# Kernel optimization log

Measured on AMD Instinct MI355X. Metric: run time of the kernel, lower is better.

The kernel has to match this reference:

```python
import jax, jax.numpy as jnp
import numpy as np

N_USERS = 100_000
N_ITEMS = 50_000
N_EDGES = 2_000_000
D = 64
ALPHA = 0.5      # tanh-blend coefficient (alpha)
NORM_2 = -1.0    # exponent on back-aggregation degree norm (args.norm_2)


def setup_inputs() -> dict:
    key = jax.random.key(0)
    k1, k2, k3, k4, k5 = jax.random.split(key, 5)
    return {
        "h_user": jax.random.normal(k1, (N_USERS, D), jnp.float32) * 0.1,
        "pretrained_feature": jax.random.normal(k2, (N_ITEMS, D), jnp.float32),
        "edge_w": jax.random.normal(k3, (N_ITEMS, 1), jnp.float32),
        "src_idx": jax.random.randint(k4, (N_EDGES,), 0, N_USERS, dtype=jnp.int32),
        "dst_idx": jax.random.randint(k5, (N_EDGES,), 0, N_ITEMS, dtype=jnp.int32),
    }


def reference(h_user, pretrained_feature, edge_w, src_idx, dst_idx):
    # HGCNLayer.forward: bidirectional copy_src+sum aggregation with degree norm,
    # tanh prompt blend and node-softmax edge weighting.
    ones = jnp.ones((N_EDGES,), h_user.dtype)

    # forward pass user -> item: rst[d] = sum_{(s,d) in E} h_user[s]
    rst = jax.ops.segment_sum(h_user[src_idx], dst_idx, num_segments=N_ITEMS)  # [N_ITEMS, D]
    deg_dst = jnp.clip(jax.ops.segment_sum(ones, dst_idx, num_segments=N_ITEMS), 1.0)

    # alpha * tanh prompt blend
    rst = rst + ALPHA * jnp.tanh(pretrained_feature)
    # edge-prompt softmax scaling (softmax over nodes; see notes)
    rst = jax.nn.softmax(edge_w, axis=0) * rst
    # in-degree^-1 normalization
    rst = rst / deg_dst[:, None]

    # backward pass item -> user: bsrc[s] = sum_{(s,d) in E} rst[d]
    bsrc = jax.ops.segment_sum(rst[dst_idx], src_idx, num_segments=N_USERS)  # [N_USERS, D]
    deg_src = jnp.clip(jax.ops.segment_sum(ones, src_idx, num_segments=N_USERS), 1.0)
    bsrc = bsrc * jnp.power(deg_src, NORM_2)[:, None]
    return bsrc
```

## Files before the change

### kernel.cpp

```cpp
#include <hip/hip_runtime.h>
#include <hip/hip_bf16.h>
#include <math.h>

#define N_USERS 100000
#define N_ITEMS 50000
#define N_EDGES 2000000
#define D 64

#define FB_BINS 98
#define BB_BINS 196
#define NBINS   (FB_BINS + BB_BINS)
#define CHUNK   2048
#define NCHUNK  ((N_EDGES + CHUNK - 1) / CHUNK)
#define FWD_WGS 782
#define BWD_WGS 1563
#define CAP     4032

__device__ __forceinline__ float blo(unsigned u) {
    union { unsigned i; float f; } c; c.i = u << 16; return c.f;
}
__device__ __forceinline__ float bhi(unsigned u) {
    union { unsigned i; float f; } c; c.i = u & 0xFFFF0000u; return c.f;
}
__device__ __forceinline__ unsigned bpack(float x, float y) {
    __hip_bfloat16 a = __float2bfloat16(x), b = __float2bfloat16(y);
    unsigned short ua = *reinterpret_cast<unsigned short*>(&a);
    unsigned short ub = *reinterpret_cast<unsigned short*>(&b);
    return (unsigned)ua | ((unsigned)ub << 16);
}

__global__ __launch_bounds__(256) void h2b_kernel(
    const float2* __restrict__ in, unsigned* __restrict__ out, int n) {
    int stride = gridDim.x * blockDim.x;
    for (int i = blockIdx.x * blockDim.x + threadIdx.x; i < n; i += stride) {
        float2 v = in[i];
        out[i] = bpack(v.x, v.y);
    }
}

__global__ __launch_bounds__(256) void hist_kernel(
    const int* __restrict__ src, const int* __restrict__ dst, int* __restrict__ gh) {
    __shared__ int h[NBINS];
    for (int i = threadIdx.x; i < NBINS; i += 256) h[i] = 0;
    __syncthreads();
    int stride = gridDim.x * blockDim.x;
    for (int e = blockIdx.x * blockDim.x + threadIdx.x; e < N_EDGES; e += stride) {
        atomicAdd(&h[dst[e] >> 9], 1);
        atomicAdd(&h[FB_BINS + (src[e] >> 9)], 1);
    }
    __syncthreads();
    for (int i = threadIdx.x; i < NBINS; i += 256) {
        int v = h[i];
        if (v) atomicAdd(&gh[i], v);
    }
}

__global__ void scan_excl(const int* __restrict__ in, int* __restrict__ out,
                          int* __restrict__ cur, int n) {
    const int T = 1024, E = 4;
    __shared__ int wsum[16];
    __shared__ int s_carry;
    if (threadIdx.x == 0) s_carry = 0;
    __syncthreads();

    int lane = threadIdx.x & 63;
    int wid  = threadIdx.x >> 6;

    for (int base = 0; base < n; base += T * E) {
        int idx0 = base + threadIdx.x * E;
        int v[E];
        int tot = 0;
#pragma unroll
        for (int e = 0; e < E; e++) {
            int i = idx0 + e;
            v[e] = (i < n) ? in[i] : 0;
            tot += v[e];
        }
        int incl = tot;
#pragma unroll
        for (int off = 1; off < 64; off <<= 1) {
            int t = __shfl_up(incl, off);
            if (lane >= off) incl += t;
        }
        if (lane == 63) wsum[wid] = incl;
        __syncthreads();
        if (wid == 0 && lane < 16) {
            int t = wsum[lane];
            int sc = t;
#pragma unroll
            for (int off = 1; off < 16; off <<= 1) {
                int u = __shfl_up(sc, off);
                if (lane >= off) sc += u;
            }
            wsum[lane] = sc - t;
        }
        __syncthreads();
        int wave_off = wsum[wid];
        int excl = s_carry + wave_off + incl - tot;
#pragma unroll
        for (int e = 0; e < E; e++) {
            int i = idx0 + e;
            if (i < n) { out[i] = excl; cur[i] = excl; }
            excl += v[e];
        }
        __syncthreads();
        if (threadIdx.x == T - 1) s_carry += wave_off + incl;
        __syncthreads();
    }
    if (threadIdx.x == 0) out[n] = s_carry;
}

__global__ __launch_bounds__(256) void binfill_kernel(
    const int* __restrict__ src, const int* __restrict__ dst,
    int* __restrict__ gcur, unsigned* __restrict__ stage) {
    __shared__ int cnt[NBINS];
    __shared__ int gbase[NBINS];
    __shared__ int lcur[NBINS];
    int c = blockIdx.x;
    int base = c * CHUNK;
    int nEdge = N_EDGES - base; if (nEdge > CHUNK) nEdge = CHUNK;

    for (int t = threadIdx.x; t < NBINS; t += 256) { cnt[t] = 0; lcur[t] = 0; }
    __syncthreads();

    int es[8], ed[8];
#pragma unroll
    for (int j = 0; j < 8; j++) {
        int k = j * 256 + threadIdx.x;
        if (k < nEdge) {
            es[j] = src[base + k];
            ed[j] = dst[base + k];
            atomicAdd(&cnt[ed[j] >> 9], 1);
            atomicAdd(&cnt[FB_BINS + (es[j] >> 9)], 1);
        } else {
            es[j] = -1;
        }
    }
    __syncthreads();
    for (int t = threadIdx.x; t < NBINS; t += 256) {
        int cv = cnt[t];
        gbase[t] = cv ? atomicAdd(&gcur[t], cv) : 0;
    }
    __syncthreads();
#pragma unroll
    for (int j = 0; j < 8; j++) {
        if (es[j] >= 0) {
            int s = es[j], d = ed[j];
            int bf = d >> 9;
            int p = atomicAdd(&lcur[bf], 1);
            stage[gbase[bf] + p] = (unsigned)s | ((unsigned)(d & 511) << 17);
            int bb = FB_BINS + (s >> 9);
            int q = atomicAdd(&lcur[bb], 1);
            stage[gbase[bb] + q] = (unsigned)d | ((unsigned)(s & 511) << 16);
        }
    }
}

__global__ void softmax_stats_kernel(const float* __restrict__ w, float* __restrict__ stats) {
    __shared__ float red[16];
    int tid = threadIdx.x, lane = tid & 63, wid = tid >> 6;

    float m = -INFINITY;
    for (int i = tid; i < N_ITEMS; i += 1024) m = fmaxf(m, w[i]);
#pragma unroll
    for (int off = 32; off; off >>= 1) m = fmaxf(m, __shfl_xor(m, off));
    if (lane == 0) red[wid] = m;
    __syncthreads();
    if (tid == 0) {
        float t = red[0];
        for (int k = 1; k < 16; k++) t = fmaxf(t, red[k]);
        red[0] = t;
    }
    __syncthreads();
    m = red[0];
    __syncthreads();

    float s = 0.f;
    for (int i = tid; i < N_ITEMS; i += 1024) s += expf(w[i] - m);
#pragma unroll
    for (int off = 32; off; off >>= 1) s += __shfl_xor(s, off);
    if (lane == 0) red[wid] = s;
    __syncthreads();
    if (tid == 0) {
        float t = 0.f;
        for (int k = 0; k < 16; k++) t += red[k];
        stats[0] = m;
        stats[1] = t;
    }
}

__global__ __launch_bounds__(512) void pass2_fwd_kernel(
    const unsigned* __restrict__ hu16, const float* __restrict__ pf,
    const float* __restrict__ edge_w, const unsigned* __restrict__ stage,
    const int* __restrict__ binoff, const float* __restrict__ stats,
    unsigned* __restrict__ rst16) {
    __shared__ int cnt[64];
    __shared__ int loc[65];
    __shared__ int lcur[64];
    __shared__ int sorted[CAP];
    int r = blockIdx.x;
    int B = r >> 3, sub = r & 7;
    int beg = binoff[B], end = binoff[B + 1];
    int tid = threadIdx.x, lane = tid & 63, wv = tid >> 6;
    int q = lane & 31, half = lane >> 5;

    if (tid < 64) { cnt[tid] = 0; lcur[tid] = 0; }
    __syncthreads();

    for (int k = beg + tid; k < end; k += 512) {
        unsigned e = stage[k];
        if ((int)(e >> 23) == sub) atomicAdd(&cnt[(e >> 17) & 63], 1);
    }
    __syncthreads();
    if (tid < 64) {
        int v = cnt[tid];
        int incl = v;
#pragma unroll
        for (int off = 1; off < 64; off <<= 1) {
            int t = __shfl_up(incl, off);
            if (tid >= off) incl += t;
        }
        loc[tid] = incl - v;
        if (tid == 63) loc[64] = incl;
    }
    __syncthreads();
    int nf = loc[64];

    float m = stats[0], ssum = stats[1];
    const float2* PF2 = (const float2*)pf;

    if (nf <= CAP) {
        for (int k = beg + tid; k < end; k += 512) {
            unsigned e = stage[k];
            if ((int)(e >> 23) == sub) {
                int il = (e >> 17) & 63;
                int p = atomicAdd(&lcur[il], 1);
                sorted[loc[il] + p] = (int)(e & 0x1FFFFu);
            }
        }
        __syncthreads();
        for (int il = wv; il < 64; il += 8) {
            int i = r * 64 + il;
            if (i >= N_ITEMS) continue;
            int a = loc[il], b = loc[il + 1];
            float ax = 0.f, ay = 0.f;
            int k = a;
            for (; k + 8 <= b; k += 8) {
                int s0 = sorted[k + half],     s1 = sorted[k + 2 + half];
                int s2 = sorted[k + 4 + half], s3 = sorted[k + 6 + half];
                unsigned u0 = hu16[(s0 << 5) + q];
                unsigned u1 = hu16[(s1 << 5) + q];
                unsigned u2 = hu16[(s2 << 5) + q];
                unsigned u3 = hu16[(s3 << 5) + q];
                ax += (blo(u0) + blo(u1)) + (blo(u2) + blo(u3));
                ay += (bhi(u0) + bhi(u1)) + (bhi(u2) + bhi(u3));
            }
            for (; k + 2 <= b; k += 2) {
                unsigned u = hu16[(sorted[k + half] << 5) + q];
                ax += blo(u); ay += bhi(u);
            }
            if (k < b && half == 0) {
                unsigned u = hu16[(sorted[k] << 5) + q];
                ax += blo(u); ay += bhi(u);
            }
            ax += __shfl_xor(ax, 32);
            ay += __shfl_xor(ay, 32);
            if (half == 0) {
                float deg = (float)(b - a);
                if (deg < 1.f) deg = 1.f;
                float sc = expf(edge_w[i] - m) / (ssum * deg);
                float2 pv = PF2[(size_t)i * 32 + q];
                float vx = (ax + 0.5f * tanhf(pv.x)) * sc;
                float vy = (ay + 0.5f * tanhf(pv.y)) * sc;
                rst16[(size_t)i * 32 + q] = bpack(vx, vy);
            }
        }
    } else {
        const unsigned short* HU = (const unsigned short*)hu16;
        for (int il = wv; il < 64; il += 8) {
            int i = r * 64 + il;
            if (i >= N_ITEMS) continue;
            unsigned want = ((unsigned)sub << 6) | (unsigned)il;
            float acc = 0.f;
            int dcount = 0;
            for (int k = beg; k < end; k++) {
                unsigned e = stage[k];
                if ((e >> 17) == want) {
                    union { unsigned u; float f; } c;
                    c.u = (unsigned)HU[(size_t)(e & 0x1FFFFu) * 64 + lane] << 16;
                    acc += c.f; dcount++;
                }
            }
            float deg = (float)dcount;
            if (deg < 1.f) deg = 1.f;
            float sc = expf(edge_w[i] - m) / (ssum * deg);
            float val = (acc + 0.5f * tanhf(pf[(size_t)i * D + lane])) * sc;
            float va = __shfl(val, 2 * q);
            float vb = __shfl(val, 2 * q + 1);
            if (half == 0) rst16[(size_t)i * 32 + q] = bpack(va, vb);
        }
    }
}

__global__ __launch_bounds__(512) void pass2_bwd_kernel(
    const unsigned* __restrict__ rst16, const unsigned* __restrict__ stage,
    const int* __restrict__ binoff, float* __restrict__ out) {
    __shared__ int cnt[64];
    __shared__ int loc[65];
    __shared__ int lcur[64];
    __shared__ int sorted[CAP];
    int r = blockIdx.x;
    int B = FB_BINS + (r >> 3), sub = r & 7;
    int beg = binoff[B], end = binoff[B + 1];
    int tid = threadIdx.x, lane = tid & 63, wv = tid >> 6;
    int q = lane & 31, half = lane >> 5;

    if (tid < 64) { cnt[tid] = 0; lcur[tid] = 0; }
    __syncthreads();

    for (int k = beg + tid; k < end; k += 512) {
        unsigned e = stage[k];
        if ((int)(e >> 22) == sub) atomicAdd(&cnt[(e >> 16) & 63], 1);
    }
    __syncthreads();
    if (tid < 64) {
        int v = cnt[tid];
        int incl = v;
#pragma unroll
        for (int off = 1; off < 64; off <<= 1) {
            int t = __shfl_up(incl, off);
            if (tid >= off) incl += t;
        }
        loc[tid] = incl - v;
        if (tid == 63) loc[64] = incl;
    }
    __syncthreads();
    int nf = loc[64];

    float2* OUT2 = (float2*)out;

    if (nf <= CAP) {
        for (int k = beg + tid; k < end; k += 512) {
            unsigned e = stage[k];
            if ((int)(e >> 22) == sub) {
                int il = (e >> 16) & 63;
                int p = atomicAdd(&lcur[il], 1);
                sorted[loc[il] + p] = (int)(e & 0xFFFFu);
            }
        }
        __syncthreads();
        for (int il = wv; il < 64; il += 8) {
            int u = r * 64 + il;
            if (u >= N_USERS) continue;
            int a = loc[il], b = loc[il + 1];
            float ax = 0.f, ay = 0.f;
            int k = a;
            for (; k + 8 <= b; k += 8) {
                int d0 = sorted[k + half],     d1 = sorted[k + 2 + half];
                int d2 = sorted[k + 4 + half], d3 = sorted[k + 6 + half];
                unsigned u0 = rst16[(d0 << 5) + q];
                unsigned u1 = rst16[(d1 << 5) + q];
                unsigned u2 = rst16[(d2 << 5) + q];
                unsigned u3 = rst16[(d3 << 5) + q];
                ax += (blo(u0) + blo(u1)) + (blo(u2) + blo(u3));
                ay += (bhi(u0) + bhi(u1)) + (bhi(u2) + bhi(u3));
            }
            for (; k + 2 <= b; k += 2) {
                unsigned e = rst16[(sorted[k + half] << 5) + q];
                ax += blo(e); ay += bhi(e);
            }
            if (k < b && half == 0) {
                unsigned e = rst16[(sorted[k] << 5) + q];
                ax += blo(e); ay += bhi(e);
            }
            ax += __shfl_xor(ax, 32);
            ay += __shfl_xor(ay, 32);
            if (half == 0) {
                float deg = (float)(b - a);
                if (deg < 1.f) deg = 1.f;
                OUT2[(size_t)u * 32 + q] = make_float2(ax / deg, ay / deg);
            }
        }
    } else {
        const unsigned short* RS = (const unsigned short*)rst16;
        for (int il = wv; il < 64; il += 8) {
            int u = r * 64 + il;
            if (u >= N_USERS) continue;
            unsigned want = ((unsigned)sub << 6) | (unsigned)il;
            float acc = 0.f;
            int dcount = 0;
            for (int k = beg; k < end; k++) {
                unsigned e = stage[k];
                if ((e >> 16) == want) {
                    union { unsigned ui; float f; } c;
                    c.ui = (unsigned)RS[(size_t)(e & 0xFFFFu) * 64 + lane] << 16;
                    acc += c.f; dcount++;
                }
            }
            float deg = (float)dcount;
            if (deg < 1.f) deg = 1.f;
            out[(size_t)u * D + lane] = acc / deg;
        }
    }
}

extern "C" void kernel_launch(void* const* d_in, const int* in_sizes, int n_in,
                              void* d_out, int out_size, void* d_ws, size_t ws_size,
                              hipStream_t stream) {
    const float* h_user = (const float*)d_in[0];
    const float* pf     = (const float*)d_in[1];
    const float* edge_w = (const float*)d_in[2];
    const int*   src    = (const int*)d_in[3];
    const int*   dst    = (const int*)d_in[4];
    float* out = (float*)d_out;

    char* p = (char*)d_ws;
    int* gh     = (int*)p;      p += sizeof(int) * NBINS;
    int* binoff = (int*)p;      p += sizeof(int) * (NBINS + 1);
    int* gcur   = (int*)p;      p += sizeof(int) * NBINS;
    unsigned* stage = (unsigned*)p; p += sizeof(unsigned) * (size_t)2 * N_EDGES;
    unsigned* hu16  = (unsigned*)p; p += sizeof(unsigned) * (size_t)N_USERS * 32;
    unsigned* rst16 = (unsigned*)p; p += sizeof(unsigned) * (size_t)N_ITEMS * 32;
    float* stats = (float*)p;   p += 2 * sizeof(float);

    hipMemsetAsync(gh, 0, sizeof(int) * NBINS, stream);

    hist_kernel<<<256, 256, 0, stream>>>(src, dst, gh);
    scan_excl<<<1, 1024, 0, stream>>>(gh, binoff, gcur, NBINS);
    binfill_kernel<<<NCHUNK, 256, 0, stream>>>(src, dst, gcur, stage);
    h2b_kernel<<<1024, 256, 0, stream>>>((const float2*)h_user, hu16, N_USERS * 32);
    softmax_stats_kernel<<<1, 1024, 0, stream>>>(edge_w, stats);
    pass2_fwd_kernel<<<FWD_WGS, 512, 0, stream>>>(hu16, pf, edge_w, stage, binoff, stats, rst16);
    pass2_bwd_kernel<<<BWD_WGS, 512, 0, stream>>>(rst16, stage, binoff, out);
}
```

Before: 348.3 us.

## Split edge bins by partner-index segment to localize gather footprint

Edge bins are subdivided by the high bits of the partner index (user segments for forward, item segments for backward), so each workgroup walks its bin one segment at a time. Accumulators for its 64 rows stay in registers across segments, which keeps the gathered rows within a smaller index window at any moment for better cache locality, and the smaller shared sorted buffer may allow more workgroups per CU. The binfill chunk grows to 16384 edges and re-reads src/dst instead of caching them in registers. The cost is more bins, more per-segment synchronisation and scan work, and more register pressure from the 8-wide accumulator arrays.

```diff
diff --git a/kernel.cpp b/kernel.cpp
--- a/kernel.cpp
+++ b/kernel.cpp
@@ -7,14 +7,17 @@
 #define N_EDGES 2000000
 #define D 64
 
-#define FB_BINS 98
-#define BB_BINS 196
-#define NBINS   (FB_BINS + BB_BINS)
-#define CHUNK   2048
-#define NCHUNK  ((N_EDGES + CHUNK - 1) / CHUNK)
+#define SEG_SH 14
+#define FSEG 8
+#define BSEG 4
+#define FB2 (98 * FSEG)
+#define BB2 (196 * BSEG)
+#define NB2 (FB2 + BB2)
+#define CHUNK 16384
+#define NCHUNK ((N_EDGES + CHUNK - 1) / CHUNK)
 #define FWD_WGS 782
 #define BWD_WGS 1563
-#define CAP     4032
+#define CAPC 1024
 
 __device__ __forceinline__ float blo(unsigned u) {
     union { unsigned i; float f; } c; c.i = u << 16; return c.f;
@@ -40,16 +43,17 @@
 
 __global__ __launch_bounds__(256) void hist_kernel(
     const int* __restrict__ src, const int* __restrict__ dst, int* __restrict__ gh) {
-    __shared__ int h[NBINS];
-    for (int i = threadIdx.x; i < NBINS; i += 256) h[i] = 0;
+    __shared__ int h[NB2];
+    for (int i = threadIdx.x; i < NB2; i += 256) h[i] = 0;
     __syncthreads();
     int stride = gridDim.x * blockDim.x;
     for (int e = blockIdx.x * blockDim.x + threadIdx.x; e < N_EDGES; e += stride) {
-        atomicAdd(&h[dst[e] >> 9], 1);
-        atomicAdd(&h[FB_BINS + (src[e] >> 9)], 1);
-    }
-    __syncthreads();
-    for (int i = threadIdx.x; i < NBINS; i += 256) {
+        int s = src[e], d = dst[e];
+        atomicAdd(&h[(d >> 9) * FSEG + (s >> SEG_SH)], 1);
+        atomicAdd(&h[FB2 + (s >> 9) * BSEG + (d >> SEG_SH)], 1);
+    }
+    __syncthreads();
+    for (int i = threadIdx.x; i < NB2; i += 256) {
         int v = h[i];
         if (v) atomicAdd(&gh[i], v);
     }
@@ -113,46 +117,34 @@
 __global__ __launch_bounds__(256) void binfill_kernel(
     const int* __restrict__ src, const int* __restrict__ dst,
     int* __restrict__ gcur, unsigned* __restrict__ stage) {
-    __shared__ int cnt[NBINS];
-    __shared__ int gbase[NBINS];
-    __shared__ int lcur[NBINS];
-    int c = blockIdx.x;
-    int base = c * CHUNK;
-    int nEdge = N_EDGES - base; if (nEdge > CHUNK) nEdge = CHUNK;
-
-    for (int t = threadIdx.x; t < NBINS; t += 256) { cnt[t] = 0; lcur[t] = 0; }
-    __syncthreads();
-
-    int es[8], ed[8];
-#pragma unroll
-    for (int j = 0; j < 8; j++) {
-        int k = j * 256 + threadIdx.x;
-        if (k < nEdge) {
-            es[j] = src[base + k];
-            ed[j] = dst[base + k];
-            atomicAdd(&cnt[ed[j] >> 9], 1);
-            atomicAdd(&cnt[FB_BINS + (es[j] >> 9)], 1);
-        } else {
-            es[j] = -1;
-        }
-    }
-    __syncthreads();
-    for (int t = threadIdx.x; t < NBINS; t += 256) {
+    __shared__ int cnt[NB2];
+    __shared__ int gbase[NB2];
+    __shared__ int lcur[NB2];
+    int base = blockIdx.x * CHUNK;
+    int nE = N_EDGES - base; if (nE > CHUNK) nE = CHUNK;
+
+    for (int t = threadIdx.x; t < NB2; t += 256) { cnt[t] = 0; lcur[t] = 0; }
+    __syncthreads();
+
+    for (int k = threadIdx.x; k < nE; k += 256) {
+        int s = src[base + k], d = dst[base + k];
+        atomicAdd(&cnt[(d >> 9) * FSEG + (s >> SEG_SH)], 1);
+        atomicAdd(&cnt[FB2 + (s >> 9) * BSEG + (d >> SEG_SH)], 1);
+    }
+    __syncthreads();
+    for (int t = threadIdx.x; t < NB2; t += 256) {
         int cv = cnt[t];
         gbase[t] = cv ? atomicAdd(&gcur[t], cv) : 0;
     }
     __syncthreads();
-#pragma unroll
-    for (int j = 0; j < 8; j++) {
-        if (es[j] >= 0) {
-            int s = es[j], d = ed[j];
-            int bf = d >> 9;
-            int p = atomicAdd(&lcur[bf], 1);
-            stage[gbase[bf] + p] = (unsigned)s | ((unsigned)(d & 511) << 17);
-            int bb = FB_BINS + (s >> 9);
-            int q = atomicAdd(&lcur[bb], 1);
-            stage[gbase[bb] + q] = (unsigned)d | ((unsigned)(s & 511) << 16);
-        }
+    for (int k = threadIdx.x; k < nE; k += 256) {
+        int s = src[base + k], d = dst[base + k];
+        int bf = (d >> 9) * FSEG + (s >> SEG_SH);
+        int p = atomicAdd(&lcur[bf], 1);
+        stage[gbase[bf] + p] = (unsigned)s | ((unsigned)(d & 511) << 17);
+        int bb = FB2 + (s >> 9) * BSEG + (d >> SEG_SH);
+        int q2 = atomicAdd(&lcur[bb], 1);
+        stage[gbase[bb] + q2] = (unsigned)d | ((unsigned)(s & 511) << 16);
     }
 }
 
@@ -197,107 +189,111 @@
     __shared__ int cnt[64];
     __shared__ int loc[65];
     __shared__ int lcur[64];
-    __shared__ int sorted[CAP];
+    __shared__ int sorted[CAPC];
     int r = blockIdx.x;
     int B = r >> 3, sub = r & 7;
-    int beg = binoff[B], end = binoff[B + 1];
     int tid = threadIdx.x, lane = tid & 63, wv = tid >> 6;
     int q = lane & 31, half = lane >> 5;
 
-    if (tid < 64) { cnt[tid] = 0; lcur[tid] = 0; }
-    __syncthreads();
-
-    for (int k = beg + tid; k < end; k += 512) {
-        unsigned e = stage[k];
-        if ((int)(e >> 23) == sub) atomicAdd(&cnt[(e >> 17) & 63], 1);
-    }
-    __syncthreads();
-    if (tid < 64) {
-        int v = cnt[tid];
-        int incl = v;
-#pragma unroll
-        for (int off = 1; off < 64; off <<= 1) {
-            int t = __shfl_up(incl, off);
-            if (tid >= off) incl += t;
-        }
-        loc[tid] = incl - v;
-        if (tid == 63) loc[64] = incl;
-    }
-    __syncthreads();
-    int nf = loc[64];
+    float ax[8], ay[8];
+    int dg[8];
+#pragma unroll
+    for (int j = 0; j < 8; j++) { ax[j] = 0.f; ay[j] = 0.f; dg[j] = 0; }
+
+    for (int seg = 0; seg < FSEG; seg++) {
+        int cbeg = binoff[B * FSEG + seg], cend = binoff[B * FSEG + seg + 1];
+        if (cbeg == cend) continue;
+        if (tid < 64) { cnt[tid] = 0; lcur[tid] = 0; }
+        __syncthreads();
+        for (int k = cbeg + tid; k < cend; k += 512) {
+            unsigned e = stage[k];
+            if ((int)(e >> 23) == sub) atomicAdd(&cnt[(e >> 17) & 63], 1);
+        }
+        __syncthreads();
+        if (tid < 64) {
+            int v = cnt[tid];
+            int incl = v;
+#pragma unroll
+            for (int off = 1; off < 64; off <<= 1) {
+                int t = __shfl_up(incl, off);
+                if (tid >= off) incl += t;
+            }
+            loc[tid] = incl - v;
+            if (tid == 63) loc[64] = incl;
+        }
+        __syncthreads();
+        int nf = loc[64];
+
+        if (nf <= CAPC) {
+            for (int k = cbeg + tid; k < cend; k += 512) {
+                unsigned e = stage[k];
+                if ((int)(e >> 23) == sub) {
+                    int il = (e >> 17) & 63;
+                    int p = atomicAdd(&lcur[il], 1);
+                    sorted[loc[il] + p] = (int)(e & 0x1FFFFu);
+                }
+            }
+            __syncthreads();
+#pragma unroll
+            for (int j = 0; j < 8; j++) {
+                int il = wv + 8 * j;
+                int a = loc[il], b = loc[il + 1];
+                dg[j] += b - a;
+                int k = a;
+                for (; k + 4 <= b; k += 4) {
+                    int s0 = sorted[k + half], s1 = sorted[k + 2 + half];
+                    unsigned u0 = hu16[(s0 << 5) + q];
+                    unsigned u1 = hu16[(s1 << 5) + q];
+                    ax[j] += blo(u0) + blo(u1);
+                    ay[j] += bhi(u0) + bhi(u1);
+                }
+                for (; k + 2 <= b; k += 2) {
+                    unsigned u = hu16[(sorted[k + half] << 5) + q];
+                    ax[j] += blo(u); ay[j] += bhi(u);
+                }
+                if (k < b && half == 0) {
+                    unsigned u = hu16[(sorted[k] << 5) + q];
+                    ax[j] += blo(u); ay[j] += bhi(u);
+                }
+            }
+            __syncthreads();
+        } else {
+#pragma unroll
+            for (int j = 0; j < 8; j++) {
+                int il = wv + 8 * j;
+                unsigned want = ((unsigned)sub << 6) | (unsigned)il;
+                for (int k = cbeg; k < cend; k++) {
+                    unsigned e = stage[k];
+                    if ((e >> 17) == want) {
+                        dg[j]++;
+                        if (half == 0) {
+                            unsigned u = hu16[((e & 0x1FFFFu) << 5) + q];
+                            ax[j] += blo(u); ay[j] += bhi(u);
+                        }
+                    }
+                }
+            }
+            __syncthreads();
+        }
+    }
 
     float m = stats[0], ssum = stats[1];
     const float2* PF2 = (const float2*)pf;
-
-    if (nf <= CAP) {
-        for (int k = beg + tid; k < end; k += 512) {
-            unsigned e = stage[k];
-            if ((int)(e >> 23) == sub) {
-                int il = (e >> 17) & 63;
-                int p = atomicAdd(&lcur[il], 1);
-                sorted[loc[il] + p] = (int)(e & 0x1FFFFu);
-            }
-        }
-        __syncthreads();
-        for (int il = wv; il < 64; il += 8) {
-            int i = r * 64 + il;
-            if (i >= N_ITEMS) continue;
-            int a = loc[il], b = loc[il + 1];
-            float ax = 0.f, ay = 0.f;
-            int k = a;
-            for (; k + 8 <= b; k += 8) {
-                int s0 = sorted[k + half],     s1 = sorted[k + 2 + half];
-                int s2 = sorted[k + 4 + half], s3 = sorted[k + 6 + half];
-                unsigned u0 = hu16[(s0 << 5) + q];
-                unsigned u1 = hu16[(s1 << 5) + q];
-                unsigned u2 = hu16[(s2 << 5) + q];
-                unsigned u3 = hu16[(s3 << 5) + q];
-                ax += (blo(u0) + blo(u1)) + (blo(u2) + blo(u3));
-                ay += (bhi(u0) + bhi(u1)) + (bhi(u2) + bhi(u3));
-            }
-            for (; k + 2 <= b; k += 2) {
-                unsigned u = hu16[(sorted[k + half] << 5) + q];
-                ax += blo(u); ay += bhi(u);
-            }
-            if (k < b && half == 0) {
-                unsigned u = hu16[(sorted[k] << 5) + q];
-                ax += blo(u); ay += bhi(u);
-            }
-            ax += __shfl_xor(ax, 32);
-            ay += __shfl_xor(ay, 32);
-            if (half == 0) {
-                float deg = (float)(b - a);
-                if (deg < 1.f) deg = 1.f;
-                float sc = expf(edge_w[i] - m) / (ssum * deg);
-                float2 pv = PF2[(size_t)i * 32 + q];
-                float vx = (ax + 0.5f * tanhf(pv.x)) * sc;
-                float vy = (ay + 0.5f * tanhf(pv.y)) * sc;
-                rst16[(size_t)i * 32 + q] = bpack(vx, vy);
-            }
-        }
-    } else {
-        const unsigned short* HU = (const unsigned short*)hu16;
-        for (int il = wv; il < 64; il += 8) {
-            int i = r * 64 + il;
-            if (i >= N_ITEMS) continue;
-            unsigned want = ((unsigned)sub << 6) | (unsigned)il;
-            float acc = 0.f;
-            int dcount = 0;
-            for (int k = beg; k < end; k++) {
-                unsigned e = stage[k];
-                if ((e >> 17) == want) {
-                    union { unsigned u; float f; } c;
-                    c.u = (unsigned)HU[(size_t)(e & 0x1FFFFu) * 64 + lane] << 16;
-                    acc += c.f; dcount++;
-                }
-            }
-            float deg = (float)dcount;
+#pragma unroll
+    for (int j = 0; j < 8; j++) {
+        int il = wv + 8 * j;
+        int i = r * 64 + il;
+        if (i >= N_ITEMS) continue;
+        ax[j] += __shfl_xor(ax[j], 32);
+        ay[j] += __shfl_xor(ay[j], 32);
+        if (half == 0) {
+            float deg = (float)dg[j];
             if (deg < 1.f) deg = 1.f;
             float sc = expf(edge_w[i] - m) / (ssum * deg);
-            float val = (acc + 0.5f * tanhf(pf[(size_t)i * D + lane])) * sc;
-            float va = __shfl(val, 2 * q);
-            float vb = __shfl(val, 2 * q + 1);
-            if (half == 0) rst16[(size_t)i * 32 + q] = bpack(va, vb);
+            float2 pv = PF2[(size_t)i * 32 + q];
+            float vx = (ax[j] + 0.5f * tanhf(pv.x)) * sc;
+            float vy = (ay[j] + 0.5f * tanhf(pv.y)) * sc;
+            rst16[(size_t)i * 32 + q] = bpack(vx, vy);
         }
     }
 }
@@ -308,98 +304,106 @@
     __shared__ int cnt[64];
     __shared__ int loc[65];
     __shared__ int lcur[64];
-    __shared__ int sorted[CAP];
+    __shared__ int sorted[CAPC];
     int r = blockIdx.x;
-    int B = FB_BINS + (r >> 3), sub = r & 7;
-    int beg = binoff[B], end = binoff[B + 1];
+    int B = r >> 3, sub = r & 7;
     int tid = threadIdx.x, lane = tid & 63, wv = tid >> 6;
     int q = lane & 31, half = lane >> 5;
 
-    if (tid < 64) { cnt[tid] = 0; lcur[tid] = 0; }
-    __syncthreads();
-
-    for (int k = beg + tid; k < end; k += 512) {
-        unsigned e = stage[k];
-        if ((int)(e >> 22) == sub) atomicAdd(&cnt[(e >> 16) & 63], 1);
-    }
-    __syncthreads();
-    if (tid < 64) {
-        int v = cnt[tid];
-        int incl = v;
-#pragma unroll
-        for (int off = 1; off < 64; off <<= 1) {
-            int t = __shfl_up(incl, off);
-            if (tid >= off) incl += t;
-        }
-        loc[tid] = incl - v;
-        if (tid == 63) loc[64] = incl;
-    }
-    __syncthreads();
-    int nf = loc[64];
+    float ax[8], ay[8];
+    int dg[8];
+#pragma unroll
+    for (int j = 0; j < 8; j++) { ax[j] = 0.f; ay[j] = 0.f; dg[j] = 0; }
+
+    for (int seg = 0; seg < BSEG; seg++) {
+        int cbeg = binoff[FB2 + B * BSEG + seg], cend = binoff[FB2 + B * BSEG + seg + 1];
+        if (cbeg == cend) continue;
+        if (tid < 64) { cnt[tid] = 0; lcur[tid] = 0; }
+        __syncthreads();
+        for (int k = cbeg + tid; k < cend; k += 512) {
+            unsigned e = stage[k];
+            if ((int)(e >> 22) == sub) atomicAdd(&cnt[(e >> 16) & 63], 1);
+        }
+        __syncthreads();
+        if (tid < 64) {
+            int v = cnt[tid];
+            int incl = v;
+#pragma unroll
+            for (int off = 1; off < 64; off <<= 1) {
+                int t = __shfl_up(incl, off);
+                if (tid >= off) incl += t;
+            }
+            loc[tid] = incl - v;
+            if (tid == 63) loc[64] = incl;
+        }
+        __syncthreads();
+        int nf = loc[64];
+
+        if (nf <= CAPC) {
+            for (int k = cbeg + tid; k < cend; k += 512) {
+                unsigned e = stage[k];
+                if ((int)(e >> 22) == sub) {
+                    int il = (e >> 16) & 63;
+                    int p = atomicAdd(&lcur[il], 1);
+                    sorted[loc[il] + p] = (int)(e & 0xFFFFu);
+                }
+            }
+            __syncthreads();
+#pragma unroll
+            for (int j = 0; j < 8; j++) {
+                int il = wv + 8 * j;
+                int a = loc[il], b = loc[il + 1];
+                dg[j] += b - a;
+                int k = a;
+                for (; k + 4 <= b; k += 4) {
+                    int d0 = sorted[k + half], d1 = sorted[k + 2 + half];
+                    unsigned u0 = rst16[(d0 << 5) + q];
+                    unsigned u1 = rst16[(d1 << 5) + q];
+                    ax[j] += blo(u0) + blo(u1);
+                    ay[j] += bhi(u0) + bhi(u1);
+                }
+                for (; k + 2 <= b; k += 2) {
+                    unsigned u = rst16[(sorted[k + half] << 5) + q];
+                    ax[j] += blo(u); ay[j] += bhi(u);
+                }
+                if (k < b && half == 0) {
+                    unsigned u = rst16[(sorted[k] << 5) + q];
+                    ax[j] += blo(u); ay[j] += bhi(u);
+                }
+            }
+            __syncthreads();
+        } else {
+#pragma unroll
+            for (int j = 0; j < 8; j++) {
+                int il = wv + 8 * j;
+                unsigned want = ((unsigned)sub << 6) | (unsigned)il;
+                for (int k = cbeg; k < cend; k++) {
+                    unsigned e = stage[k];
+                    if ((e >> 16) == want) {
+                        dg[j]++;
+                        if (half == 0) {
+                            unsigned u = rst16[((e & 0xFFFFu) << 5) + q];
+                            ax[j] += blo(u); ay[j] += bhi(u);
+                        }
+                    }
+                }
+            }
+            __syncthreads();
+        }
+    }
 
     float2* OUT2 = (float2*)out;
-
-    if (nf <= CAP) {
-        for (int k = beg + tid; k < end; k += 512) {
-            unsigned e = stage[k];
-            if ((int)(e >> 22) == sub) {
-                int il = (e >> 16) & 63;
-                int p = atomicAdd(&lcur[il], 1);
-                sorted[loc[il] + p] = (int)(e & 0xFFFFu);
-            }
-        }
-        __syncthreads();
-        for (int il = wv; il < 64; il += 8) {
-            int u = r * 64 + il;
-            if (u >= N_USERS) continue;
-            int a = loc[il], b = loc[il + 1];
-            float ax = 0.f, ay = 0.f;
-            int k = a;
-            for (; k + 8 <= b; k += 8) {
-                int d0 = sorted[k + half],     d1 = sorted[k + 2 + half];
-                int d2 = sorted[k + 4 + half], d3 = sorted[k + 6 + half];
-                unsigned u0 = rst16[(d0 << 5) + q];
-                unsigned u1 = rst16[(d1 << 5) + q];
-                unsigned u2 = rst16[(d2 << 5) + q];
-                unsigned u3 = rst16[(d3 << 5) + q];
-                ax += (blo(u0) + blo(u1)) + (blo(u2) + blo(u3));
-                ay += (bhi(u0) + bhi(u1)) + (bhi(u2) + bhi(u3));
-            }
-            for (; k + 2 <= b; k += 2) {
-                unsigned e = rst16[(sorted[k + half] << 5) + q];
-                ax += blo(e); ay += bhi(e);
-            }
-            if (k < b && half == 0) {
-                unsigned e = rst16[(sorted[k] << 5) + q];
-                ax += blo(e); ay += bhi(e);
-            }
-            ax += __shfl_xor(ax, 32);
-            ay += __shfl_xor(ay, 32);
-            if (half == 0) {
-                float deg = (float)(b - a);
-                if (deg < 1.f) deg = 1.f;
-                OUT2[(size_t)u * 32 + q] = make_float2(ax / deg, ay / deg);
-            }
-        }
-    } else {
-        const unsigned short* RS = (const unsigned short*)rst16;
-        for (int il = wv; il < 64; il += 8) {
-            int u = r * 64 + il;
-            if (u >= N_USERS) continue;
-            unsigned want = ((unsigned)sub << 6) | (unsigned)il;
-            float acc = 0.f;
-            int dcount = 0;
-            for (int k = beg; k < end; k++) {
-                unsigned e = stage[k];
-                if ((e >> 16) == want) {
-                    union { unsigned ui; float f; } c;
-                    c.ui = (unsigned)RS[(size_t)(e & 0xFFFFu) * 64 + lane] << 16;
-                    acc += c.f; dcount++;
-                }
-            }
-            float deg = (float)dcount;
+#pragma unroll
+    for (int j = 0; j < 8; j++) {
+        int il = wv + 8 * j;
+        int u = r * 64 + il;
+        if (u >= N_USERS) continue;
+        ax[j] += __shfl_xor(ax[j], 32);
+        ay[j] += __shfl_xor(ay[j], 32);
+        if (half == 0) {
+            float deg = (float)dg[j];
             if (deg < 1.f) deg = 1.f;
-            out[(size_t)u * D + lane] = acc / deg;
+            OUT2[(size_t)u * 32 + q] = make_float2(ax[j] / deg, ay[j] / deg);
         }
     }
 }
@@ -415,18 +419,18 @@
     float* out = (float*)d_out;
 
     char* p = (char*)d_ws;
-    int* gh     = (int*)p;      p += sizeof(int) * NBINS;
-    int* binoff = (int*)p;      p += sizeof(int) * (NBINS + 1);
-    int* gcur   = (int*)p;      p += sizeof(int) * NBINS;
+    int* gh     = (int*)p;      p += sizeof(int) * NB2;
+    int* binoff = (int*)p;      p += sizeof(int) * (NB2 + 1);
+    int* gcur   = (int*)p;      p += sizeof(int) * NB2;
     unsigned* stage = (unsigned*)p; p += sizeof(unsigned) * (size_t)2 * N_EDGES;
     unsigned* hu16  = (unsigned*)p; p += sizeof(unsigned) * (size_t)N_USERS * 32;
     unsigned* rst16 = (unsigned*)p; p += sizeof(unsigned) * (size_t)N_ITEMS * 32;
     float* stats = (float*)p;   p += 2 * sizeof(float);
 
-    hipMemsetAsync(gh, 0, sizeof(int) * NBINS, stream);
+    hipMemsetAsync(gh, 0, sizeof(int) * NB2, stream);
 
     hist_kernel<<<256, 256, 0, stream>>>(src, dst, gh);
-    scan_excl<<<1, 1024, 0, stream>>>(gh, binoff, gcur, NBINS);
+    scan_excl<<<1, 1024, 0, stream>>>(gh, binoff, gcur, NB2);
     binfill_kernel<<<NCHUNK, 256, 0, stream>>>(src, dst, gcur, stage);
     h2b_kernel<<<1024, 256, 0, stream>>>((const float2*)h_user, hu16, N_USERS * 32);
     softmax_stats_kernel<<<1, 1024, 0, stream>>>(edge_w, stats);
```

Result: slower. 366.7 us (+5.3%).
